# Optimization experiments

Measured on AMD Instinct MI355X. Metric: run time of the kernel, lower is better.

## Reference

```python
import jax, jax.numpy as jnp
import numpy as np

B, T, N, F_IN = 2, 4, 1024, 256
H, N_HIDDEN = 8, 128
SLOPE = 0.2
NEG_INF = -9e16


def setup_inputs() -> dict:
    key = jax.random.key(0)
    k1, k2, k3, k4 = jax.random.split(key, 4)
    h = jax.random.normal(k1, (B, T, N, F_IN), dtype=jnp.float32)
    adj_mat = jax.random.randint(k2, (N, N), 0, 2, dtype=jnp.int32)
    W = jax.random.normal(k3, (F_IN, H * N_HIDDEN), dtype=jnp.float32) * 0.05
    a = jax.random.normal(k4, (H, 2 * N_HIDDEN, 1), dtype=jnp.float32) * 0.05
    return {"h": h, "adj_mat": adj_mat, "W": W, "a": a}


def reference(h, adj_mat, W, a):
    b, t, n, _ = h.shape
    # linear transform: [B,T,N,F_in] @ [F_in, H*nh] -> [B,T,N,H*nh]
    ht = jnp.einsum('btjs,sh->btjh', h, W)
    # dropout is identity in eval mode
    ht = ht.reshape(b, t, n, H, N_HIDDEN).transpose(0, 1, 3, 2, 4)  # [B,T,H,N,nh]
    # additive attention scores
    a_src = a[:, :N_HIDDEN, :]   # [H, nh, 1]
    a_tgt = a[:, N_HIDDEN:, :]   # [H, nh, 1]
    src = jnp.einsum('bthnd,hdo->bthno', ht, a_src)  # [B,T,H,N,1]
    tgt = jnp.einsum('bthnd,hdo->bthno', ht, a_tgt)  # [B,T,H,N,1]
    e = src + jnp.swapaxes(tgt, -1, -2)              # [B,T,H,N,N]
    e = jnp.where(e >= 0, e, SLOPE * e)              # LeakyReLU
    e = jnp.where(adj_mat > 0, e, jnp.float32(NEG_INF))
    attention = jax.nn.softmax(e, axis=-1)
    # weighted aggregation: [B,T,H,N,N] @ [B,T,H,N,nh]
    h_prime = jnp.einsum('bthij,bthjd->bthid', attention, ht)
    # concat=False branch: mean over dim 0 (batch), as in the source
    return h_prime.mean(axis=0)  # [T,H,N,nh]
```

## Files before the change

### kernel.cpp

```cpp
#include <hip/hip_runtime.h>
#include <cstddef>
#include <cstdint>

#define B_ 2
#define T_ 4
#define N_ 1024
#define FIN_ 256
#define H_ 8
#define D_ 128
#define L2E_ 1.4426950408889634f

typedef __attribute__((ext_vector_type(8))) short short8;
typedef __attribute__((ext_vector_type(4))) float f32x4;

#define MFMA16(A, B, C) __builtin_amdgcn_mfma_f32_16x16x32_bf16((A), (B), (C), 0, 0, 0)

__device__ __forceinline__ unsigned short f2bf(float f) {
    uint32_t u = __float_as_uint(f);
    uint32_t r = (u + 0x7fffu + ((u >> 16) & 1u)) >> 16;
    return (unsigned short)r;
}

__device__ __forceinline__ uint32_t cvt_pk_bf16(float lo, float hi) {
    uint32_t r;
    asm volatile("v_cvt_pk_bf16_f32 %0, %1, %2" : "=v"(r) : "v"(lo), "v"(hi));
    return r;
}

__device__ __forceinline__ float fexp2(float x) {
#if __has_builtin(__builtin_amdgcn_exp2f)
    return __builtin_amdgcn_exp2f(x);
#else
    float r;
    asm("v_exp_f32 %0, %1" : "=v"(r) : "v"(x));
    return r;
#endif
}

__device__ __forceinline__ void load_lds16(const unsigned short* g, unsigned short* l) {
    __builtin_amdgcn_global_load_lds(
        (const __attribute__((address_space(1))) uint32_t*)g,
        (__attribute__((address_space(3))) uint32_t*)l, 16, 0, 0);
}

__global__ __launch_bounds__(256) void k_prep(const int* __restrict__ adj,
                                              const float* __restrict__ W,
                                              const float* __restrict__ a,
                                              unsigned short* __restrict__ Wt_bf,
                                              uint32_t* __restrict__ adjbits,
                                              float* __restrict__ wa) {
    __shared__ float wl[64][68];
    const int bid = blockIdx.x, tid = threadIdx.x;
    if (bid < 128) {
        const int w = bid * 256 + tid;
        const int i = w >> 5, jw = w & 31;
        const int4* p = (const int4*)(adj + (size_t)i * N_ + jw * 32);
        uint32_t bits = 0;
        #pragma unroll
        for (int q = 0; q < 8; ++q) {
            const int4 v = p[q];
            bits |= (uint32_t)(v.x > 0) << (q * 4 + 0);
            bits |= (uint32_t)(v.y > 0) << (q * 4 + 1);
            bits |= (uint32_t)(v.z > 0) << (q * 4 + 2);
            bits |= (uint32_t)(v.w > 0) << (q * 4 + 3);
        }
        adjbits[w] = bits;
    } else if (bid < 192) {
        const int tb  = bid - 128;
        const int hk0 = (tb >> 2) * 64;
        const int s0  = (tb & 3) * 64;
        {
            const int r  = tid >> 2;
            const int c0 = (tid & 3) * 16;
            #pragma unroll
            for (int k = 0; k < 4; ++k)
                *(float4*)&wl[r][c0 + k * 4] =
                    *(const float4*)(W + (size_t)(s0 + r) * (H_ * D_) + hk0 + c0 + k * 4);
        }
        __syncthreads();
        {
            const int r2 = tid >> 2;
            const int c2 = (tid & 3) * 16;
            unsigned short ob[16];
            #pragma unroll
            for (int k = 0; k < 16; ++k) ob[k] = f2bf(wl[c2 + k][r2]);
            unsigned short* dst = Wt_bf + (size_t)(hk0 + r2) * FIN_ + s0 + c2;
            *(uint4*)(dst)     = *(uint4*)&ob[0];
            *(uint4*)(dst + 8) = *(uint4*)&ob[8];
        }
    } else {
        const int o    = (bid - 192) * 256 + tid;
        const int head = o >> 9;
        const int st   = (o >> 8) & 1;
        const int s    = o & 255;
        const float* wr = W + (size_t)s * (H_ * D_) + head * D_;
        const float* ar = a + head * 256 + st * 128;
        float sum = 0.f;
        #pragma unroll
        for (int d = 0; d < 128; d += 4) {
            const float4 wv = *(const float4*)(wr + d);
            const float4 av = *(const float4*)(ar + d);
            sum += wv.x * av.x + wv.y * av.y + wv.z * av.z + wv.w * av.w;
        }
        wa[s * 16 + head * 2 + st] = sum;
    }
}

__global__ __launch_bounds__(256, 2) void k_gemm_sp(const float* __restrict__ h,
                                                    const unsigned short* __restrict__ Wt_bf,
                                                    const float* __restrict__ wa,
                                                    unsigned short* __restrict__ htT,
                                                    float* __restrict__ s1, float* __restrict__ s2,
                                                    float* __restrict__ t1, float* __restrict__ t2) {
    __shared__ __align__(16) char smem[24576];
    const int bid = blockIdx.x, tid = threadIdx.x;
    if (bid < 1024) {
        unsigned short* a_lds = (unsigned short*)smem;
        unsigned short* b_lds = (unsigned short*)(smem + 16384);
        const int xcd  = bid & 7;
        const int slot = bid >> 3;
        const int gid  = xcd * 8 + (slot >> 4);
        const int bt   = gid >> 3;
        const int n0   = (gid & 7) * 128;
        const int hk0  = (slot & 15) * 64;
        const int w = tid >> 6, lane = tid & 63;
        const int row16 = lane & 15, kgrp = lane >> 4;
        const int kswz = (kgrp ^ ((row16 >> 1) & 3)) * 8;
        const int ar  = tid >> 1;
        const int akh = tid & 1;
        const int asub = ar >> 4, arow = ar & 15;
        const int ax = (arow >> 1) & 3;
        const int aslot0 = ((akh * 2) ^ ax) * 8;
        const int aslot1 = ((akh * 2 + 1) ^ ax) * 8;
        const float* ga = h + ((size_t)bt * N_ + n0 + ar) * FIN_ + akh * 16;
        unsigned short* aw_ = a_lds + asub * 512 + arow * 32;
        const int brow = lane >> 2;
        const int bsb  = (lane & 3) ^ ((lane >> 3) & 3);
        const unsigned short* gb = Wt_bf + (size_t)(hk0 + w * 16 + brow) * FIN_ + bsb * 8;
        unsigned short* bw_ = b_lds + w * 512 + (size_t)lane * 8;

        float4 rf0, rf1, rf2, rf3;

#define LOADA(KS) {                                                            \
        const float* g = ga + (KS) * 32;                                       \
        rf0 = *(const float4*)(g);      rf1 = *(const float4*)(g + 4);         \
        rf2 = *(const float4*)(g + 8);  rf3 = *(const float4*)(g + 12); }

#define WRITEA(BUF) {                                                          \
        uint4 o0, o1;                                                          \
        o0.x = cvt_pk_bf16(rf0.x, rf0.y); o0.y = cvt_pk_bf16(rf0.z, rf0.w);    \
        o0.z = cvt_pk_bf16(rf1.x, rf1.y); o0.w = cvt_pk_bf16(rf1.z, rf1.w);    \
        o1.x = cvt_pk_bf16(rf2.x, rf2.y); o1.y = cvt_pk_bf16(rf2.z, rf2.w);    \
        o1.z = cvt_pk_bf16(rf3.x, rf3.y); o1.w = cvt_pk_bf16(rf3.z, rf3.w);    \
        unsigned short* ad = aw_ + (BUF) * 4096;                               \
        *(uint4*)(ad + aslot0) = o0;                                           \
        *(uint4*)(ad + aslot1) = o1; }

#define COMPK(BUF) {                                                           \
        const unsigned short* ab = a_lds + (BUF) * 4096;                       \
        const short8 bfv = *(const short8*)(b_lds + (BUF) * 2048 + w * 512 + row16 * 32 + kswz); \
        _Pragma("unroll")                                                      \
        for (int nt = 0; nt < 8; ++nt) {                                       \
            const short8 afv = *(const short8*)(ab + nt * 512 + row16 * 32 + kswz); \
            acc[nt] = MFMA16(afv, bfv, acc[nt]);                               \
        } }

        f32x4 acc[8];
        #pragma unroll
        for (int nt = 0; nt < 8; ++nt) acc[nt] = (f32x4){0.f, 0.f, 0.f, 0.f};

        LOADA(0)
        WRITEA(0)
        load_lds16(gb, bw_);
        LOADA(1)
        asm volatile("s_waitcnt vmcnt(4) lgkmcnt(0)" ::: "memory");
        __builtin_amdgcn_s_barrier();

        for (int ks = 0; ks < 8; ++ks) {
            const int cur = ks & 1;
            WRITEA(cur ^ 1)
            load_lds16(gb + ((ks + 1) & 7) * 32, bw_ + (cur ^ 1) * 2048);
            LOADA((ks + 2) & 7)
            COMPK(cur)
            asm volatile("s_waitcnt vmcnt(4) lgkmcnt(0)" ::: "memory");
            __builtin_amdgcn_s_barrier();
        }
#undef LOADA
#undef WRITEA
#undef COMPK
        const int hk   = hk0 + w * 16 + row16;
        const int head = hk >> 7;
        const int d    = hk & 127;
        unsigned short* ob = htT + ((size_t)(bt * H_ + head) * D_ + d) * N_;
        #pragma unroll
        for (int nt = 0; nt < 8; ++nt) {
            ushort4 v;
            v.x = f2bf(acc[nt][0]); v.y = f2bf(acc[nt][1]);
            v.z = f2bf(acc[nt][2]); v.w = f2bf(acc[nt][3]);
            *(ushort4*)(ob + n0 + nt * 16 + kgrp * 4) = v;
        }
    } else {
        float (*was)[16] = (float(*)[16])smem;
        {
            const int f = tid * 16;
            #pragma unroll
            for (int k = 0; k < 4; ++k)
                *(float4*)&was[f >> 4][k * 4] = *(const float4*)(wa + f + k * 4);
        }
        __syncthreads();
        const int r = tid >> 2, q = tid & 3;
        const int R = (bid - 1024) * 64 + r;
        const float* hrow = h + (size_t)R * FIN_ + q * 64;
        float acc[16];
        #pragma unroll
        for (int o = 0; o < 16; ++o) acc[o] = 0.f;
        for (int k = 0; k < 64; k += 4) {
            const float4 hv = *(const float4*)(hrow + k);
            const int s = q * 64 + k;
            #pragma unroll
            for (int kk = 0; kk < 4; ++kk) {
                const float hs = (kk == 0) ? hv.x : (kk == 1) ? hv.y : (kk == 2) ? hv.z : hv.w;
                #pragma unroll
                for (int o = 0; o < 16; ++o) acc[o] += hs * was[s + kk][o];
            }
        }
        #pragma unroll
        for (int o = 0; o < 16; ++o) {
            acc[o] += __shfl_xor(acc[o], 1);
            acc[o] += __shfl_xor(acc[o], 2);
        }
        const int bt = R >> 10, n = R & 1023;
        #pragma unroll
        for (int k = 0; k < 4; ++k) {
            const int o = q * 4 + k;
            const int head = o >> 1;
            const size_t idx = ((size_t)(bt * H_ + head)) * N_ + n;
            const float v = acc[o];
            if (o & 1) { t1[idx] = v * L2E_; t2[idx] = v * (0.2f * L2E_); }
            else       { s1[idx] = v * L2E_; s2[idx] = v * (0.2f * L2E_); }
        }
    }
}

struct SC {
    float4 a1l, a1h, a2l, a2h;
    uint32_t mA, mB;
};

__global__ __launch_bounds__(256, 2) void k_attn(const unsigned short* __restrict__ htT,
                                                 const float* __restrict__ s1,
                                                 const float* __restrict__ s2,
                                                 const float* __restrict__ t1,
                                                 const float* __restrict__ t2,
                                                 const uint32_t* __restrict__ adjbits,
                                                 float* __restrict__ out) {
    __shared__ __align__(16) char smem[65536];
    unsigned short* stg = (unsigned short*)smem;
    const int xcd  = blockIdx.x & 7;
    const int slot = blockIdx.x >> 3;
    const int th   = xcd * 4 + (slot >> 4);
    const int i0   = (slot & 15) * 64;
    const int tid = threadIdx.x;
    const int w = tid >> 6, lane = tid & 63;
    const int b = w & 1, isub = w >> 1;
    const int row16 = lane & 15, kgrp = lane >> 4, jrel = kgrp * 8;
    const int kswz = (kgrp ^ ((row16 >> 1) & 3)) * 8;
    const int bth = b * (T_ * H_) + th;
    const int iA  = i0 + isub * 32 + row16;
    const int iB  = iA + 16;
    const float s1A = s1[(size_t)bth * N_ + iA], s2A = s2[(size_t)bth * N_ + iA];
    const float s1B = s1[(size_t)bth * N_ + iB], s2B = s2[(size_t)bth * N_ + iB];
    const float* t1b = t1 + (size_t)bth * N_;
    const float* t2b = t2 + (size_t)bth * N_;
    const uint32_t* adjA = adjbits + (size_t)iA * (N_ / 32);
    const uint32_t* adjB = adjbits + (size_t)iB * (N_ / 32);

    const int sb  = w >> 1;
    const int sd0 = (w & 1) * 64 + (lane >> 2);
    const int sj  = ((lane & 3) ^ ((lane >> 3) & 3)) * 8;
    const unsigned short* gstg = htT + ((size_t)(sb * (T_ * H_) + th) * D_ + sd0) * N_ + sj;
    unsigned short* lstg = stg + (size_t)w * 2048 + (size_t)lane * 8;

#define STAGE(BUF, T32) {                                        \
        const unsigned short* gs = gstg + (size_t)(T32) * 32;    \
        unsigned short* ls = lstg + (BUF) * 8192;                \
        load_lds16(gs,           ls);                            \
        load_lds16(gs + 16 * N_, ls + 512);                      \
        load_lds16(gs + 32 * N_, ls + 1024);                     \
        load_lds16(gs + 48 * N_, ls + 1536); }

#define LOADSC(S, T32) {                                         \
        S.a1l = *(const float4*)(t1b + (T32) * 32 + jrel);       \
        S.a1h = *(const float4*)(t1b + (T32) * 32 + jrel + 4);   \
        S.a2l = *(const float4*)(t2b + (T32) * 32 + jrel);       \
        S.a2h = *(const float4*)(t2b + (T32) * 32 + jrel + 4);   \
        S.mA  = adjA[(T32)];                                     \
        S.mB  = adjB[(T32)]; }

    f32x4 accA[8], accB[8];
    #pragma unroll
    for (int nt = 0; nt < 8; ++nt) {
        accA[nt] = (f32x4){0.f, 0.f, 0.f, 0.f};
        accB[nt] = (f32x4){0.f, 0.f, 0.f, 0.f};
    }
    f32x4 daccA = (f32x4){0.f, 0.f, 0.f, 0.f};
    f32x4 daccB = (f32x4){0.f, 0.f, 0.f, 0.f};
    short8 ones8;
    {
        const short ov = (row16 == 0) ? (short)0x3F80 : (short)0;
        #pragma unroll
        for (int e = 0; e < 8; ++e) ones8[e] = ov;
    }
    const unsigned short* rdbase = stg + b * 4096 + row16 * 32 + kswz;

    SC scA, scB;

#define SUBP(BUFIDX, SCS, TNEXT)                                               \
    {                                                                          \
        const float tj1[8] = {SCS.a1l.x, SCS.a1l.y, SCS.a1l.z, SCS.a1l.w,      \
                              SCS.a1h.x, SCS.a1h.y, SCS.a1h.z, SCS.a1h.w};     \
        const float tj2[8] = {SCS.a2l.x, SCS.a2l.y, SCS.a2l.z, SCS.a2l.w,      \
                              SCS.a2h.x, SCS.a2h.y, SCS.a2h.z, SCS.a2h.w};     \
        const uint32_t mA = SCS.mA >> jrel;                                    \
        const uint32_t mB = SCS.mB >> jrel;                                    \
        float wvA[8], wvB[8];                                                  \
        _Pragma("unroll")                                                      \
        for (int e = 0; e < 8; ++e) {                                          \
            const float eA = fmaxf(s1A + tj1[e], s2A + tj2[e]);                \
            const float eB = fmaxf(s1B + tj1[e], s2B + tj2[e]);                \
            wvA[e] = ((mA >> e) & 1u) ? fexp2(eA) : 0.f;                       \
            wvB[e] = ((mB >> e) & 1u) ? fexp2(eB) : 0.f;                       \
        }                                                                      \
        short8 afA, afB;                                                       \
        _Pragma("unroll")                                                      \
        for (int p = 0; p < 4; ++p) {                                          \
            ((uint32_t*)&afA)[p] = cvt_pk_bf16(wvA[2 * p], wvA[2 * p + 1]);    \
            ((uint32_t*)&afB)[p] = cvt_pk_bf16(wvB[2 * p], wvB[2 * p + 1]);    \
        }                                                                      \
        LOADSC(SCS, (TNEXT))                                                   \
        const unsigned short* rb = rdbase + (BUFIDX) * 8192;                   \
        short8 bfr[8];                                                         \
        _Pragma("unroll")                                                      \
        for (int nt = 0; nt < 8; ++nt) bfr[nt] = *(const short8*)(rb + nt * 512); \
        _Pragma("unroll")                                                      \
        for (int nt = 0; nt < 8; ++nt) {                                       \
            accA[nt] = MFMA16(afA, bfr[nt], accA[nt]);                         \
            accB[nt] = MFMA16(afB, bfr[nt], accB[nt]);                         \
        }                                                                      \
        daccA = MFMA16(afA, ones8, daccA);                                     \
        daccB = MFMA16(afB, ones8, daccB);                                     \
    }

    STAGE(0, 0)
    STAGE(1, 1)
    LOADSC(scA, 0)
    LOADSC(scB, 1)

    for (int T = 0; T < 16; ++T) {
        const int pair  = T & 1;
        const int npair = pair ^ 1;
        asm volatile("s_waitcnt vmcnt(12)" ::: "memory");
        __builtin_amdgcn_s_barrier();
        asm volatile("" ::: "memory");
        STAGE(npair * 2,     (2 * T + 2) & 31)
        STAGE(npair * 2 + 1, (2 * T + 3) & 31)
        SUBP(pair * 2,     scA, (2 * T + 2) & 31)
        SUBP(pair * 2 + 1, scB, (2 * T + 3) & 31)
    }
#undef SUBP
#undef LOADSC
#undef STAGE

    __syncthreads();

    float ivA[4], ivB[4];
    #pragma unroll
    for (int r = 0; r < 4; ++r) {
        ivA[r] = __shfl(1.0f / daccA[r], kgrp * 16);
        ivB[r] = __shfl(1.0f / daccB[r], kgrp * 16);
    }

    float* comb = (float*)smem;
    if (b == 1) {
        #pragma unroll
        for (int nt = 0; nt < 8; ++nt)
            #pragma unroll
            for (int r = 0; r < 4; ++r) {
                const int il = isub * 32 + kgrp * 4 + r;
                const int d  = nt * 16 + row16;
                comb[il * 128 + d]        = accA[nt][r] * ivA[r];
                comb[(il + 16) * 128 + d] = accB[nt][r] * ivB[r];
            }
    }
    __syncthreads();
    if (b == 0) {
        #pragma unroll
        for (int nt = 0; nt < 8; ++nt)
            #pragma unroll
            for (int r = 0; r < 4; ++r) {
                const int il = isub * 32 + kgrp * 4 + r;
                const int d  = nt * 16 + row16;
                out[((size_t)th * N_ + i0 + il) * D_ + d] =
                    0.5f * (accA[nt][r] * ivA[r] + comb[il * 128 + d]);
                out[((size_t)th * N_ + i0 + il + 16) * D_ + d] =
                    0.5f * (accB[nt][r] * ivB[r] + comb[(il + 16) * 128 + d]);
            }
    }
}

extern "C" void kernel_launch(void* const* d_in, const int* in_sizes, int n_in,
                              void* d_out, int out_size, void* d_ws, size_t ws_size,
                              hipStream_t stream) {
    const float* h   = (const float*)d_in[0];
    const int*   adj = (const int*)d_in[1];
    const float* W   = (const float*)d_in[2];
    const float* a   = (const float*)d_in[3];
    float* out = (float*)d_out;

    char* p = (char*)d_ws;
    unsigned short* htT = (unsigned short*)p;  p += (size_t)B_ * T_ * H_ * D_ * N_ * 2;
    float* s1 = (float*)p;                     p += (size_t)B_ * T_ * H_ * N_ * 4;
    float* s2 = (float*)p;                     p += (size_t)B_ * T_ * H_ * N_ * 4;
    float* t1 = (float*)p;                     p += (size_t)B_ * T_ * H_ * N_ * 4;
    float* t2 = (float*)p;                     p += (size_t)B_ * T_ * H_ * N_ * 4;
    uint32_t* adjbits = (uint32_t*)p;          p += (size_t)N_ * N_ / 32 * 4;
    unsigned short* Wt_bf = (unsigned short*)p;p += (size_t)(H_ * D_) * FIN_ * 2;
    float* wa = (float*)p;

    k_prep<<<dim3(208), dim3(256), 0, stream>>>(adj, W, a, Wt_bf, adjbits, wa);
    k_gemm_sp<<<dim3(1152), dim3(256), 0, stream>>>(h, Wt_bf, wa, htT, s1, s2, t1, t2);
    k_attn<<<dim3(512), dim3(256), 0, stream>>>(htT, s1, s2, t1, t2, adjbits, out);
}
```

Baseline: 77.13 us.

## Use 16-bit lane masks for adjacency and compute LeakyReLU scaling in-kernel

The adjacency bitmask is replaced by a per-element 16-bit mask (0xFFFF or 0) packed two per word. This lets the attention kernel AND it directly onto the packed bf16 exponentials instead of shifting and selecting bit by bit. The precomputed 0.2-scaled score arrays s2/t2 are dropped, and LeakyReLU is recomputed with packed float2 multiply and max. This removes per-element select logic and two score loads per tile, but the adjacency mask buffer grows 16x, raising global/L2 traffic in the attention loop. The vmcnt wait count is adjusted to match the changed number of outstanding loads.

```diff
diff --git a/kernel.cpp b/kernel.cpp
--- a/kernel.cpp
+++ b/kernel.cpp
@@ -12,6 +12,7 @@
 
 typedef __attribute__((ext_vector_type(8))) short short8;
 typedef __attribute__((ext_vector_type(4))) float f32x4;
+typedef __attribute__((ext_vector_type(2))) float f32x2;
 
 #define MFMA16(A, B, C) __builtin_amdgcn_mfma_f32_16x16x32_bf16((A), (B), (C), 0, 0, 0)
 
@@ -47,26 +48,22 @@
                                               const float* __restrict__ W,
                                               const float* __restrict__ a,
                                               unsigned short* __restrict__ Wt_bf,
-                                              uint32_t* __restrict__ adjbits,
+                                              uint32_t* __restrict__ adjm,
                                               float* __restrict__ wa) {
     __shared__ float wl[64][68];
     const int bid = blockIdx.x, tid = threadIdx.x;
-    if (bid < 128) {
-        const int w = bid * 256 + tid;
-        const int i = w >> 5, jw = w & 31;
-        const int4* p = (const int4*)(adj + (size_t)i * N_ + jw * 32);
-        uint32_t bits = 0;
-        #pragma unroll
-        for (int q = 0; q < 8; ++q) {
-            const int4 v = p[q];
-            bits |= (uint32_t)(v.x > 0) << (q * 4 + 0);
-            bits |= (uint32_t)(v.y > 0) << (q * 4 + 1);
-            bits |= (uint32_t)(v.z > 0) << (q * 4 + 2);
-            bits |= (uint32_t)(v.w > 0) << (q * 4 + 3);
-        }
-        adjbits[w] = bits;
-    } else if (bid < 192) {
-        const int tb  = bid - 128;
+    if (bid < 512) {
+        const int w0 = (bid * 256 + tid) * 4;
+        const int4 p0 = *(const int4*)(adj + (size_t)w0 * 2);
+        const int4 p1 = *(const int4*)(adj + (size_t)w0 * 2 + 4);
+        uint4 m;
+        m.x = (p0.x > 0 ? 0xFFFFu : 0u) | (p0.y > 0 ? 0xFFFF0000u : 0u);
+        m.y = (p0.z > 0 ? 0xFFFFu : 0u) | (p0.w > 0 ? 0xFFFF0000u : 0u);
+        m.z = (p1.x > 0 ? 0xFFFFu : 0u) | (p1.y > 0 ? 0xFFFF0000u : 0u);
+        m.w = (p1.z > 0 ? 0xFFFFu : 0u) | (p1.w > 0 ? 0xFFFF0000u : 0u);
+        *(uint4*)(adjm + w0) = m;
+    } else if (bid < 576) {
+        const int tb  = bid - 512;
         const int hk0 = (tb >> 2) * 64;
         const int s0  = (tb & 3) * 64;
         {
@@ -89,7 +86,7 @@
             *(uint4*)(dst + 8) = *(uint4*)&ob[8];
         }
     } else {
-        const int o    = (bid - 192) * 256 + tid;
+        const int o    = (bid - 576) * 256 + tid;
         const int head = o >> 9;
         const int st   = (o >> 8) & 1;
         const int s    = o & 255;
@@ -110,8 +107,8 @@
                                                     const unsigned short* __restrict__ Wt_bf,
                                                     const float* __restrict__ wa,
                                                     unsigned short* __restrict__ htT,
-                                                    float* __restrict__ s1, float* __restrict__ s2,
-                                                    float* __restrict__ t1, float* __restrict__ t2) {
+                                                    float* __restrict__ s1,
+                                                    float* __restrict__ t1) {
     __shared__ __align__(16) char smem[24576];
     const int bid = blockIdx.x, tid = threadIdx.x;
     if (bid < 1024) {
@@ -235,24 +232,22 @@
             const int o = q * 4 + k;
             const int head = o >> 1;
             const size_t idx = ((size_t)(bt * H_ + head)) * N_ + n;
-            const float v = acc[o];
-            if (o & 1) { t1[idx] = v * L2E_; t2[idx] = v * (0.2f * L2E_); }
-            else       { s1[idx] = v * L2E_; s2[idx] = v * (0.2f * L2E_); }
+            const float v = acc[o] * L2E_;
+            if (o & 1) t1[idx] = v;
+            else       s1[idx] = v;
         }
     }
 }
 
 struct SC {
-    float4 a1l, a1h, a2l, a2h;
-    uint32_t mA, mB;
+    float4 a1l, a1h;
+    uint4  m4A, m4B;
 };
 
 __global__ __launch_bounds__(256, 2) void k_attn(const unsigned short* __restrict__ htT,
                                                  const float* __restrict__ s1,
-                                                 const float* __restrict__ s2,
                                                  const float* __restrict__ t1,
-                                                 const float* __restrict__ t2,
-                                                 const uint32_t* __restrict__ adjbits,
+                                                 const uint32_t* __restrict__ adjm,
                                                  float* __restrict__ out) {
     __shared__ __align__(16) char smem[65536];
     unsigned short* stg = (unsigned short*)smem;
@@ -268,12 +263,13 @@
     const int bth = b * (T_ * H_) + th;
     const int iA  = i0 + isub * 32 + row16;
     const int iB  = iA + 16;
-    const float s1A = s1[(size_t)bth * N_ + iA], s2A = s2[(size_t)bth * N_ + iA];
-    const float s1B = s1[(size_t)bth * N_ + iB], s2B = s2[(size_t)bth * N_ + iB];
+    const float s1A = s1[(size_t)bth * N_ + iA];
+    const float s1B = s1[(size_t)bth * N_ + iB];
+    const f32x2 s1A2 = {s1A, s1A}, s1B2 = {s1B, s1B};
+    const f32x2 c02  = {0.2f, 0.2f};
     const float* t1b = t1 + (size_t)bth * N_;
-    const float* t2b = t2 + (size_t)bth * N_;
-    const uint32_t* adjA = adjbits + (size_t)iA * (N_ / 32);
-    const uint32_t* adjB = adjbits + (size_t)iB * (N_ / 32);
+    const uint32_t* amA = adjm + (size_t)iA * (N_ / 2);
+    const uint32_t* amB = adjm + (size_t)iB * (N_ / 2);
 
     const int sb  = w >> 1;
     const int sd0 = (w & 1) * 64 + (lane >> 2);
@@ -292,10 +288,8 @@
 #define LOADSC(S, T32) {                                         \
         S.a1l = *(const float4*)(t1b + (T32) * 32 + jrel);       \
         S.a1h = *(const float4*)(t1b + (T32) * 32 + jrel + 4);   \
-        S.a2l = *(const float4*)(t2b + (T32) * 32 + jrel);       \
-        S.a2h = *(const float4*)(t2b + (T32) * 32 + jrel + 4);   \
-        S.mA  = adjA[(T32)];                                     \
-        S.mB  = adjB[(T32)]; }
+        S.m4A = *(const uint4*)(amA + (T32) * 16 + kgrp * 4);    \
+        S.m4B = *(const uint4*)(amB + (T32) * 16 + kgrp * 4); }
 
     f32x4 accA[8], accB[8];
     #pragma unroll
@@ -317,25 +311,23 @@
 
 #define SUBP(BUFIDX, SCS, TNEXT)                                               \
     {                                                                          \
-        const float tj1[8] = {SCS.a1l.x, SCS.a1l.y, SCS.a1l.z, SCS.a1l.w,      \
-                              SCS.a1h.x, SCS.a1h.y, SCS.a1h.z, SCS.a1h.w};     \
-        const float tj2[8] = {SCS.a2l.x, SCS.a2l.y, SCS.a2l.z, SCS.a2l.w,      \
-                              SCS.a2h.x, SCS.a2h.y, SCS.a2h.z, SCS.a2h.w};     \
-        const uint32_t mA = SCS.mA >> jrel;                                    \
-        const uint32_t mB = SCS.mB >> jrel;                                    \
-        float wvA[8], wvB[8];                                                  \
-        _Pragma("unroll")                                                      \
-        for (int e = 0; e < 8; ++e) {                                          \
-            const float eA = fmaxf(s1A + tj1[e], s2A + tj2[e]);                \
-            const float eB = fmaxf(s1B + tj1[e], s2B + tj2[e]);                \
-            wvA[e] = ((mA >> e) & 1u) ? fexp2(eA) : 0.f;                       \
-            wvB[e] = ((mB >> e) & 1u) ? fexp2(eB) : 0.f;                       \
-        }                                                                      \
+        const f32x2 tq[4] = {{SCS.a1l.x, SCS.a1l.y}, {SCS.a1l.z, SCS.a1l.w},   \
+                             {SCS.a1h.x, SCS.a1h.y}, {SCS.a1h.z, SCS.a1h.w}};  \
+        const uint32_t mAw[4] = {SCS.m4A.x, SCS.m4A.y, SCS.m4A.z, SCS.m4A.w};  \
+        const uint32_t mBw[4] = {SCS.m4B.x, SCS.m4B.y, SCS.m4B.z, SCS.m4B.w};  \
         short8 afA, afB;                                                       \
         _Pragma("unroll")                                                      \
         for (int p = 0; p < 4; ++p) {                                          \
-            ((uint32_t*)&afA)[p] = cvt_pk_bf16(wvA[2 * p], wvA[2 * p + 1]);    \
-            ((uint32_t*)&afB)[p] = cvt_pk_bf16(wvB[2 * p], wvB[2 * p + 1]);    \
+            const f32x2 eA  = s1A2 + tq[p];                                    \
+            const f32x2 eB  = s1B2 + tq[p];                                    \
+            const f32x2 eA2 = eA * c02;                                        \
+            const f32x2 eB2 = eB * c02;                                        \
+            const float wA0 = fexp2(fmaxf(eA[0], eA2[0]));                     \
+            const float wA1 = fexp2(fmaxf(eA[1], eA2[1]));                     \
+            const float wB0 = fexp2(fmaxf(eB[0], eB2[0]));                     \
+            const float wB1 = fexp2(fmaxf(eB[1], eB2[1]));                     \
+            ((uint32_t*)&afA)[p] = cvt_pk_bf16(wA0, wA1) & mAw[p];             \
+            ((uint32_t*)&afB)[p] = cvt_pk_bf16(wB0, wB1) & mBw[p];             \
         }                                                                      \
         LOADSC(SCS, (TNEXT))                                                   \
         const unsigned short* rb = rdbase + (BUFIDX) * 8192;                   \
@@ -359,7 +351,7 @@
     for (int T = 0; T < 16; ++T) {
         const int pair  = T & 1;
         const int npair = pair ^ 1;
-        asm volatile("s_waitcnt vmcnt(12)" ::: "memory");
+        asm volatile("s_waitcnt vmcnt(8)" ::: "memory");
         __builtin_amdgcn_s_barrier();
         asm volatile("" ::: "memory");
         STAGE(npair * 2,     (2 * T + 2) & 31)
@@ -420,14 +412,12 @@
     char* p = (char*)d_ws;
     unsigned short* htT = (unsigned short*)p;  p += (size_t)B_ * T_ * H_ * D_ * N_ * 2;
     float* s1 = (float*)p;                     p += (size_t)B_ * T_ * H_ * N_ * 4;
-    float* s2 = (float*)p;                     p += (size_t)B_ * T_ * H_ * N_ * 4;
     float* t1 = (float*)p;                     p += (size_t)B_ * T_ * H_ * N_ * 4;
-    float* t2 = (float*)p;                     p += (size_t)B_ * T_ * H_ * N_ * 4;
-    uint32_t* adjbits = (uint32_t*)p;          p += (size_t)N_ * N_ / 32 * 4;
+    uint32_t* adjm = (uint32_t*)p;             p += (size_t)N_ * N_ / 2 * 4;
     unsigned short* Wt_bf = (unsigned short*)p;p += (size_t)(H_ * D_) * FIN_ * 2;
     float* wa = (float*)p;
 
-    k_prep<<<dim3(208), dim3(256), 0, stream>>>(adj, W, a, Wt_bf, adjbits, wa);
-    k_gemm_sp<<<dim3(1152), dim3(256), 0, stream>>>(h, Wt_bf, wa, htT, s1, s2, t1, t2);
-    k_attn<<<dim3(512), dim3(256), 0, stream>>>(htT, s1, s2, t1, t2, adjbits, out);
-}
+    k_prep<<<dim3(592), dim3(256), 0, stream>>>(adj, W, a, Wt_bf, adjm, wa);
+    k_gemm_sp<<<dim3(1152), dim3(256), 0, stream>>>(h, Wt_bf, wa, htT, s1, t1);
+    k_attn<<<dim3(512), dim3(256), 0, stream>>>(htT, s1, t1, adjm, out);
+}
```

Result: faster. 73.20 us (-5.1%).
